# Optimization experiments

Hardware: AMD Instinct MI355X
Metric: run time of the kernel (lower is better)

## Reference

```python
import jax, jax.numpy as jnp
import numpy as np

KERNEL_MUL = 2.0
KERNEL_NUM = 5


def setup_inputs() -> dict:
    key = jax.random.key(0)
    k1, k2 = jax.random.split(key)
    N, D = 4096, 256
    source = jax.random.normal(k1, (N, D), dtype=jnp.float32)
    target = jax.random.normal(k2, (N, D), dtype=jnp.float32)
    return {"source": source, "target": target}


def _gaussian_kernel_sum(source, target):
    # total: [2N, D]
    total = jnp.concatenate([source, target], axis=0)
    n = total.shape[0]
    sq = jnp.sum(total * total, axis=1)  # [2N]
    L2 = sq[:, None] + sq[None, :] - 2.0 * (total @ total.T)  # [2N, 2N]
    # Bandwidth from detached mean of off-diagonal-normalized sum (torch uses .data)
    bandwidth = jax.lax.stop_gradient(jnp.sum(L2)) / (n * n - n)
    bandwidth = bandwidth / (KERNEL_MUL ** (KERNEL_NUM // 2))
    kernels = sum(
        jnp.exp(-L2 / (bandwidth * (KERNEL_MUL ** i))) for i in range(KERNEL_NUM)
    )
    return kernels


def reference(source, target):
    b = source.shape[0]
    K = _gaussian_kernel_sum(source, target)
    XX = jnp.mean(K[:b, :b])
    YY = jnp.mean(K[b:, b:])
    XY = jnp.mean(K[:b, b:])
    YX = jnp.mean(K[b:, :b])
    return XX + YY - XY - YX
```

## Files before the change

kernel.cpp:

```cpp
#include <hip/hip_runtime.h>


#define NROWS 8192
#define HALF  4096
#define DIM   256
#define CONVB 256
#define NTILE 2080
#define GRIDP 512

typedef float f32x4 __attribute__((ext_vector_type(4)));
typedef float f32x2 __attribute__((ext_vector_type(2)));

__device__ __forceinline__ const float* row_ptr(const float* src, const float* tgt, int r) {
    return (r < HALF) ? (src + (size_t)r * DIM) : (tgt + (size_t)(r - HALF) * DIM);
}

__device__ __forceinline__ void gload_lds16(const void* g, void* l) {
    __builtin_amdgcn_global_load_lds(
        (const __attribute__((address_space(1))) unsigned int*)g,
        (__attribute__((address_space(3))) unsigned int*)l, 16, 0, 0);
}

__device__ __forceinline__ void stage_panel(const ulonglong2* plane, int P,
                                            ulonglong2* lds, int w, int lane) {
    #pragma unroll
    for (int i = 0; i < 8; ++i) {
        int k = w + 4 * i;
        int u = k >> 1;
        int h = k & 1;
        int rg = (h * 64 + lane) ^ ((u & 3) << 1);
        gload_lds16(plane + (size_t)P * 2048 + (size_t)u * 128 + rg,
                    lds + u * 128 + h * 64);
    }
}

__global__ __launch_bounds__(256) void k_conv(const float* __restrict__ src,
                                              const float* __restrict__ tgt,
                                              unsigned char* __restrict__ hi,
                                              float* __restrict__ sq,
                                              float* __restrict__ part,
                                              double* __restrict__ parts1,
                                              float* __restrict__ outacc,
                                              unsigned int* __restrict__ cnt,
                                              float* __restrict__ out) {
    __shared__ __align__(16) unsigned char sh8[32 * 256];
    __shared__ float4 cs[4][64];
    __shared__ double s1s[4];

    int w = threadIdx.x >> 6, lane = threadIdx.x & 63;
    int r0 = blockIdx.x * 32;

    float4 v[8];
    #pragma unroll
    for (int i = 0; i < 8; ++i) {
        int row = r0 + w * 8 + i;
        v[i] = ((const float4*)row_ptr(src, tgt, row))[lane];
    }

    if (blockIdx.x == 0) {
        if (threadIdx.x < 8) outacc[threadIdx.x] = 0.0f;
        if (threadIdx.x == 0) { *cnt = 0u; out[0] = 0.0f; }
    }

    float4 csum = {0.f, 0.f, 0.f, 0.f};
    double s1w = 0.0;
    #pragma unroll
    for (int i = 0; i < 8; ++i) {
        int rl  = w * 8 + i;
        float xs[4] = {v[i].x, v[i].y, v[i].z, v[i].w};
        int pk = __builtin_amdgcn_cvt_pk_fp8_f32(xs[0], xs[1], 0, false);
        pk     = __builtin_amdgcn_cvt_pk_fp8_f32(xs[2], xs[3], pk, true);
        int o  = lane >> 1, h = lane & 1;
        *(int*)&sh8[rl * 256 + (((o ^ rl) & 31) << 3) + (h << 2)] = pk;
        csum.x += xs[0]; csum.y += xs[1]; csum.z += xs[2]; csum.w += xs[3];
        float sf = xs[0]*xs[0] + xs[1]*xs[1] + xs[2]*xs[2] + xs[3]*xs[3];
        float q0 = __builtin_amdgcn_cvt_f32_fp8(pk, 0);
        float q1 = __builtin_amdgcn_cvt_f32_fp8(pk, 1);
        float q2 = __builtin_amdgcn_cvt_f32_fp8(pk, 2);
        float q3 = __builtin_amdgcn_cvt_f32_fp8(pk, 3);
        float sQ = q0*q0 + q1*q1 + q2*q2 + q3*q3;
        #pragma unroll
        for (int off = 32; off; off >>= 1) {
            sf += __shfl_xor(sf, off, 64);
            sQ += __shfl_xor(sQ, off, 64);
        }
        if (lane == 0) { sq[r0 + rl] = sQ; s1w += (double)sf; }
    }
    __syncthreads();
    int panel = blockIdx.x >> 2, quarter = blockIdx.x & 3;
    #pragma unroll
    for (int c = threadIdx.x; c < 512; c += 256) {
        int u = c >> 5, rl = c & 31;
        int tt = u >> 2, j = u & 3;
        int o0 = 8 * tt + j;
        int o1 = 8 * tt + 4 + j;
        unsigned long long q0 = *(const unsigned long long*)
            &sh8[rl * 256 + (((o0 ^ rl) & 31) << 3)];
        unsigned long long q1 = *(const unsigned long long*)
            &sh8[rl * 256 + (((o1 ^ rl) & 31) << 3)];
        ulonglong2 q = {q0, q1};
        size_t goff = ((size_t)panel * 2048 + (size_t)u * 128 + quarter * 32 + rl);
        ((ulonglong2*)hi)[goff] = q;
    }
    cs[w][lane] = csum;
    if (lane == 0) s1s[w] = s1w;
    __syncthreads();
    if (w == 0) {
        float4 a = cs[0][lane], b = cs[1][lane], c = cs[2][lane], d = cs[3][lane];
        float4 tot = {a.x + b.x + c.x + d.x, a.y + b.y + c.y + d.y,
                      a.z + b.z + c.z + d.z, a.w + b.w + c.w + d.w};
        *(float4*)&part[(size_t)blockIdx.x * DIM + lane * 4] = tot;
        if (lane == 0) parts1[blockIdx.x] = s1s[0] + s1s[1] + s1s[2] + s1s[3];
    }
}

__global__ __launch_bounds__(256, 2) void k_pairs(const unsigned char* __restrict__ hi,
                                                  const float* __restrict__ sq,
                                                  const float* __restrict__ part,
                                                  const double* __restrict__ parts1,
                                                  float* __restrict__ outacc,
                                                  unsigned int* __restrict__ cnt,
                                                  float* __restrict__ out) {
    __shared__ __align__(16) ulonglong2 ldsA[2048];
    __shared__ __align__(16) ulonglong2 ldsB[2048];
    __shared__ float wsum[4];
    __shared__ double shd[256];

    int bid = blockIdx.x;
    int t0 = (bid * NTILE) / GRIDP;
    int t1 = ((bid + 1) * NTILE) / GRIDP;

    int id = t0, I = 0;
    for (;;) {
        int c = 64 - I;
        if (id < c) break;
        id -= c; ++I;
    }
    int J = I + id;

    int t    = threadIdx.x;
    int lane = t & 63;
    int w    = t >> 6;
    int lr   = lane & 15, lq = lane >> 4;
    int wr   = w >> 1, wc = w & 1;
    int lrx  = lr ^ (lq << 1);

    const ulonglong2* plane = (const ulonglong2*)hi;

    stage_panel(plane, I, ldsA, w, lane);
    if (J != I) stage_panel(plane, J, ldsB, w, lane);

    shd[t] = parts1[t];
    __syncthreads();
    for (int off = 128; off; off >>= 1) {
        if (t < off) shd[t] += shd[t + off];
        __syncthreads();
    }
    double S1 = shd[0];
    __syncthreads();
    {
        float c0 = 0.f, c1 = 0.f, c2 = 0.f, c3 = 0.f;
        #pragma unroll 16
        for (int b = 0; b < CONVB; b += 4) {
            c0 += part[(b + 0) * DIM + t];
            c1 += part[(b + 1) * DIM + t];
            c2 += part[(b + 2) * DIM + t];
            c3 += part[(b + 3) * DIM + t];
        }
        double c = (double)((c0 + c1) + (c2 + c3));
        shd[t] = c * c;
    }
    __syncthreads();
    for (int off = 128; off; off >>= 1) {
        if (t < off) shd[t] += shd[t + off];
        __syncthreads();
    }
    double S2    = shd[0];
    double nd    = (double)NROWS;
    double sumL2 = 2.0 * nd * S1 - 2.0 * S2;
    double bw    = sumL2 / (nd * nd - nd) / 4.0;
    float  s     = (float)(-1.0 / (16.0 * bw * 0.69314718055994530942));
    f32x2  m2s   = {-2.0f * s, -2.0f * s};

    asm volatile("s_waitcnt vmcnt(0)");
    __syncthreads();

    float wtot = 0.0f;
    int curI = I, curJ = J;

    #pragma unroll 1
    for (int tile = t0; tile < t1; ++tile) {
        const ulonglong2* lB  = (curJ == curI) ? ldsA : ldsB;
        const ulonglong2* pAl = ldsA + lq * 128 + wr * 64 + lrx;
        const ulonglong2* pBl = lB   + lq * 128 + wc * 64 + lrx;

        ulonglong2 fA[4][4], fB[4][4];
        #pragma unroll
        for (int tt = 0; tt < 4; ++tt) {
            #pragma unroll
            for (int m = 0; m < 4; ++m) fA[tt][m] = pAl[tt * 512 + m * 16];
            #pragma unroll
            for (int n = 0; n < 4; ++n) fB[tt][n] = pBl[tt * 512 + n * 16];
        }
        __syncthreads();

        int nI = curI, nJ = curJ + 1;
        if (nJ == 64) { nI = curI + 1; nJ = nI; }
        if (tile + 1 < t1) {
            if (nI != curI) stage_panel(plane, nI, ldsA, w, lane);
            else            stage_panel(plane, nJ, ldsB, w, lane);
        }

        f32x4 acc[4][4];
        #pragma unroll
        for (int m = 0; m < 4; ++m)
            #pragma unroll
            for (int n = 0; n < 4; ++n) acc[m][n] = (f32x4){0.f, 0.f, 0.f, 0.f};
        #pragma unroll
        for (int tt = 0; tt < 4; ++tt) {
            #pragma unroll
            for (int m = 0; m < 4; ++m)
                #pragma unroll
                for (int n = 0; n < 4; ++n)
                    acc[m][n] = __builtin_amdgcn_mfma_f32_16x16x32_fp8_fp8(
                        (long)fA[tt][m].x, (long)fB[tt][n].x, acc[m][n], 0, 0, 0);
            #pragma unroll
            for (int m = 0; m < 4; ++m)
                #pragma unroll
                for (int n = 0; n < 4; ++n)
                    acc[m][n] = __builtin_amdgcn_mfma_f32_16x16x32_fp8_fp8(
                        (long)fA[tt][m].y, (long)fB[tt][n].y, acc[m][n], 0, 0, 0);
        }

        float wgt = (curJ == curI) ? 1.0f : 2.0f;
        float sgn = ((curI < 32) == (curJ < 32)) ? 1.0f : -1.0f;
        int ro_eff = curI * 128 + wr * 64;
        int co_eff = curJ * 128 + wc * 64;
        float4 sqa4[4];
        float  sqbv[4];
        #pragma unroll
        for (int m = 0; m < 4; ++m) sqa4[m] = *(const float4*)&sq[ro_eff + m * 16 + lq * 4];
        #pragma unroll
        for (int n = 0; n < 4; ++n) sqbv[n] = s * sq[co_eff + n * 16 + lr];

        f32x2 ssa01[4], ssa23[4];
        #pragma unroll
        for (int m = 0; m < 4; ++m) {
            ssa01[m] = (f32x2){s * sqa4[m].x, s * sqa4[m].y};
            ssa23[m] = (f32x2){s * sqa4[m].z, s * sqa4[m].w};
        }

        f32x2 acc0 = {0.f, 0.f}, acc1 = {0.f, 0.f};
        #pragma unroll
        for (int m = 0; m < 4; ++m) {
            #pragma unroll
            for (int n = 0; n < 4; ++n) {
                f32x2 sbn = {sqbv[n], sqbv[n]};
                f32x2 a01 = {acc[m][n][0], acc[m][n][1]};
                f32x2 a23 = {acc[m][n][2], acc[m][n][3]};
                f32x2 e01 = (ssa01[m] + sbn) + m2s * a01;
                f32x2 e23 = (ssa23[m] + sbn) + m2s * a23;
                f32x2 u01, u23;
                u01.x = __builtin_amdgcn_exp2f(e01.x);
                u01.y = __builtin_amdgcn_exp2f(e01.y);
                u23.x = __builtin_amdgcn_exp2f(e23.x);
                u23.y = __builtin_amdgcn_exp2f(e23.y);
                f32x2 p2a = u01 * u01, p4a = p2a * p2a, p8a = p4a * p4a, p16a = p8a * p8a;
                f32x2 p2b = u23 * u23, p4b = p2b * p2b, p8b = p4b * p4b, p16b = p8b * p8b;
                acc0 += ((u01 + p2a) + (p4a + p8a)) + p16a;
                acc1 += ((u23 + p2b) + (p4b + p8b)) + p16b;
            }
        }
        wtot += ((acc0.x + acc0.y) + (acc1.x + acc1.y)) * sgn * wgt;

        asm volatile("s_waitcnt vmcnt(0)");
        __syncthreads();
        curI = nI; curJ = nJ;
    }

    #pragma unroll
    for (int off = 32; off; off >>= 1) wtot += __shfl_xor(wtot, off, 64);
    if (lane == 0) wsum[w] = wtot;
    __syncthreads();
    if (t == 0) {
        float tot = (wsum[0] + wsum[1] + wsum[2] + wsum[3])
                  * (1.0f / ((float)HALF * (float)HALF));
        float r = atomicAdd(&outacc[bid & 7], tot);
        asm volatile("" :: "v"(r) : "memory");
        unsigned prev = atomicAdd(cnt, 1u);
        if (prev == (unsigned)(GRIDP - 1)) {
            float total = 0.0f;
            #pragma unroll
            for (int k2 = 0; k2 < 8; ++k2) total += atomicAdd(&outacc[k2], 0.0f);
            out[0] = total;
        }
    }
}

extern "C" void kernel_launch(void* const* d_in, const int* in_sizes, int n_in,
                              void* d_out, int out_size, void* d_ws, size_t ws_size,
                              hipStream_t stream) {
    const float* src = (const float*)d_in[0];
    const float* tgt = (const float*)d_in[1];
    float* out = (float*)d_out;

    char* ws = (char*)d_ws;
    unsigned int* cnt = (unsigned int*)(ws + 0);
    float*  outacc = (float*)(ws + 64);
    float*  sq     = (float*)(ws + 128);
    float*  part   = (float*)(ws + 33024);
    double* parts1 = (double*)(ws + 295424);
    unsigned char* hi = (unsigned char*)(ws + 297472);

    k_conv <<<CONVB, 256, 0, stream>>>(src, tgt, hi, sq, part, parts1,
                                       outacc, cnt, out);
    k_pairs<<<GRIDP, 256, 0, stream>>>(hi, sq, part, parts1, outacc, cnt, out);
}
```

Before: 96.40 us.

## Software-pipeline MFMA of next tile with exp epilogue of previous tile

Restructures the tile loop so the fp8 MFMA matrix products for the current tile are interleaved with the exp-sum epilogue of the previous tile, using double accumulators (accA/accB) with a prologue and an epilogue. The aim is to overlap matrix-core work with VALU transcendental work, which previously ran back to back. Fragment loads are also split per k-step instead of loading all fragments up front. The cost is doubled accumulator register pressure (two 16x f32x4 sets), which may lower occupancy or cause spills.

```diff
diff --git a/kernel.cpp b/kernel.cpp
--- a/kernel.cpp
+++ b/kernel.cpp
@@ -187,79 +187,159 @@
 
     float wtot = 0.0f;
     int curI = I, curJ = J;
-
-    #pragma unroll 1
-    for (int tile = t0; tile < t1; ++tile) {
+    int pI = 0, pJ = 0;
+
+    f32x4 accA[4][4], accB[4][4];
+
+    {
         const ulonglong2* lB  = (curJ == curI) ? ldsA : ldsB;
         const ulonglong2* pAl = ldsA + lq * 128 + wr * 64 + lrx;
         const ulonglong2* pBl = lB   + lq * 128 + wc * 64 + lrx;
-
-        ulonglong2 fA[4][4], fB[4][4];
         #pragma unroll
         for (int tt = 0; tt < 4; ++tt) {
-            #pragma unroll
-            for (int m = 0; m < 4; ++m) fA[tt][m] = pAl[tt * 512 + m * 16];
-            #pragma unroll
-            for (int n = 0; n < 4; ++n) fB[tt][n] = pBl[tt * 512 + n * 16];
-        }
-        __syncthreads();
-
+            ulonglong2 fA[4], fB[4];
+            #pragma unroll
+            for (int m = 0; m < 4; ++m) fA[m] = pAl[tt * 512 + m * 16];
+            #pragma unroll
+            for (int n = 0; n < 4; ++n) fB[n] = pBl[tt * 512 + n * 16];
+            #pragma unroll
+            for (int m = 0; m < 4; ++m)
+                #pragma unroll
+                for (int n = 0; n < 4; ++n) {
+                    f32x4 c0 = (tt == 0) ? (f32x4){0.f,0.f,0.f,0.f} : accA[m][n];
+                    accA[m][n] = __builtin_amdgcn_mfma_f32_16x16x32_fp8_fp8(
+                        (long)fA[m].x, (long)fB[n].x, c0, 0, 0, 0);
+                }
+            #pragma unroll
+            for (int m = 0; m < 4; ++m)
+                #pragma unroll
+                for (int n = 0; n < 4; ++n)
+                    accA[m][n] = __builtin_amdgcn_mfma_f32_16x16x32_fp8_fp8(
+                        (long)fA[m].y, (long)fB[n].y, accA[m][n], 0, 0, 0);
+        }
+        __syncthreads();
+        int nI = curI, nJ = curJ + 1;
+        if (nJ == 64) { nI = curI + 1; nJ = nI; }
+        if (t0 + 1 < t1) {
+            if (nI != curI) stage_panel(plane, nI, ldsA, w, lane);
+            else            stage_panel(plane, nJ, ldsB, w, lane);
+        }
+        pI = curI; pJ = curJ; curI = nI; curJ = nJ;
+    }
+
+    #pragma unroll 1
+    for (int tile = t0 + 1; tile < t1; ++tile) {
+        asm volatile("s_waitcnt vmcnt(0)");
+        __syncthreads();
+
+        const ulonglong2* lB  = (curJ == curI) ? ldsA : ldsB;
+        const ulonglong2* pAl = ldsA + lq * 128 + wr * 64 + lrx;
+        const ulonglong2* pBl = lB   + lq * 128 + wc * 64 + lrx;
+
+        float pwgt = (pJ == pI) ? 1.0f : 2.0f;
+        float psgn = ((pI < 32) == (pJ < 32)) ? 1.0f : -1.0f;
+        int pro = pI * 128 + wr * 64;
+        int pco = pJ * 128 + wc * 64;
+        float4 sqa4[4];
+        float  psqbv[4];
+        #pragma unroll
+        for (int m = 0; m < 4; ++m) sqa4[m] = *(const float4*)&sq[pro + m * 16 + lq * 4];
+        #pragma unroll
+        for (int n = 0; n < 4; ++n) psqbv[n] = s * sq[pco + n * 16 + lr];
+        f32x2 pssa01[4], pssa23[4];
+        #pragma unroll
+        for (int m = 0; m < 4; ++m) {
+            pssa01[m] = (f32x2){s * sqa4[m].x, s * sqa4[m].y};
+            pssa23[m] = (f32x2){s * sqa4[m].z, s * sqa4[m].w};
+        }
+        f32x2 eac0 = {0.f, 0.f}, eac1 = {0.f, 0.f};
+
+        #pragma unroll
+        for (int tt = 0; tt < 4; ++tt) {
+            ulonglong2 fA[4], fB[4];
+            #pragma unroll
+            for (int m = 0; m < 4; ++m) fA[m] = pAl[tt * 512 + m * 16];
+            #pragma unroll
+            for (int n = 0; n < 4; ++n) fB[n] = pBl[tt * 512 + n * 16];
+            {
+                f32x2 sa01 = pssa01[tt], sa23 = pssa23[tt];
+                #pragma unroll
+                for (int n = 0; n < 4; ++n) {
+                    f32x2 sbn = {psqbv[n], psqbv[n]};
+                    f32x2 a01 = {accA[tt][n][0], accA[tt][n][1]};
+                    f32x2 a23 = {accA[tt][n][2], accA[tt][n][3]};
+                    f32x2 e01 = (sa01 + sbn) + m2s * a01;
+                    f32x2 e23 = (sa23 + sbn) + m2s * a23;
+                    f32x2 u01, u23;
+                    u01.x = __builtin_amdgcn_exp2f(e01.x);
+                    u01.y = __builtin_amdgcn_exp2f(e01.y);
+                    u23.x = __builtin_amdgcn_exp2f(e23.x);
+                    u23.y = __builtin_amdgcn_exp2f(e23.y);
+                    f32x2 p2a = u01 * u01, p4a = p2a * p2a, p8a = p4a * p4a, p16a = p8a * p8a;
+                    f32x2 p2b = u23 * u23, p4b = p2b * p2b, p8b = p4b * p4b, p16b = p8b * p8b;
+                    eac0 += ((u01 + p2a) + (p4a + p8a)) + p16a;
+                    eac1 += ((u23 + p2b) + (p4b + p8b)) + p16b;
+                }
+            }
+            #pragma unroll
+            for (int m = 0; m < 4; ++m)
+                #pragma unroll
+                for (int n = 0; n < 4; ++n) {
+                    f32x4 c0 = (tt == 0) ? (f32x4){0.f,0.f,0.f,0.f} : accB[m][n];
+                    accB[m][n] = __builtin_amdgcn_mfma_f32_16x16x32_fp8_fp8(
+                        (long)fA[m].x, (long)fB[n].x, c0, 0, 0, 0);
+                }
+            #pragma unroll
+            for (int m = 0; m < 4; ++m)
+                #pragma unroll
+                for (int n = 0; n < 4; ++n)
+                    accB[m][n] = __builtin_amdgcn_mfma_f32_16x16x32_fp8_fp8(
+                        (long)fA[m].y, (long)fB[n].y, accB[m][n], 0, 0, 0);
+        }
+        wtot += ((eac0.x + eac0.y) + (eac1.x + eac1.y)) * psgn * pwgt;
+
+        __syncthreads();
         int nI = curI, nJ = curJ + 1;
         if (nJ == 64) { nI = curI + 1; nJ = nI; }
         if (tile + 1 < t1) {
             if (nI != curI) stage_panel(plane, nI, ldsA, w, lane);
             else            stage_panel(plane, nJ, ldsB, w, lane);
         }
-
-        f32x4 acc[4][4];
         #pragma unroll
         for (int m = 0; m < 4; ++m)
             #pragma unroll
-            for (int n = 0; n < 4; ++n) acc[m][n] = (f32x4){0.f, 0.f, 0.f, 0.f};
-        #pragma unroll
-        for (int tt = 0; tt < 4; ++tt) {
-            #pragma unroll
-            for (int m = 0; m < 4; ++m)
-                #pragma unroll
-                for (int n = 0; n < 4; ++n)
-                    acc[m][n] = __builtin_amdgcn_mfma_f32_16x16x32_fp8_fp8(
-                        (long)fA[tt][m].x, (long)fB[tt][n].x, acc[m][n], 0, 0, 0);
-            #pragma unroll
-            for (int m = 0; m < 4; ++m)
-                #pragma unroll
-                for (int n = 0; n < 4; ++n)
-                    acc[m][n] = __builtin_amdgcn_mfma_f32_16x16x32_fp8_fp8(
-                        (long)fA[tt][m].y, (long)fB[tt][n].y, acc[m][n], 0, 0, 0);
-        }
-
-        float wgt = (curJ == curI) ? 1.0f : 2.0f;
-        float sgn = ((curI < 32) == (curJ < 32)) ? 1.0f : -1.0f;
-        int ro_eff = curI * 128 + wr * 64;
-        int co_eff = curJ * 128 + wc * 64;
+            for (int n = 0; n < 4; ++n) accA[m][n] = accB[m][n];
+        pI = curI; pJ = curJ; curI = nI; curJ = nJ;
+    }
+
+    {
+        float pwgt = (pJ == pI) ? 1.0f : 2.0f;
+        float psgn = ((pI < 32) == (pJ < 32)) ? 1.0f : -1.0f;
+        int pro = pI * 128 + wr * 64;
+        int pco = pJ * 128 + wc * 64;
         float4 sqa4[4];
-        float  sqbv[4];
-        #pragma unroll
-        for (int m = 0; m < 4; ++m) sqa4[m] = *(const float4*)&sq[ro_eff + m * 16 + lq * 4];
-        #pragma unroll
-        for (int n = 0; n < 4; ++n) sqbv[n] = s * sq[co_eff + n * 16 + lr];
-
-        f32x2 ssa01[4], ssa23[4];
+        float  psqbv[4];
+        #pragma unroll
+        for (int m = 0; m < 4; ++m) sqa4[m] = *(const float4*)&sq[pro + m * 16 + lq * 4];
+        #pragma unroll
+        for (int n = 0; n < 4; ++n) psqbv[n] = s * sq[pco + n * 16 + lr];
+        f32x2 pssa01[4], pssa23[4];
         #pragma unroll
         for (int m = 0; m < 4; ++m) {
-            ssa01[m] = (f32x2){s * sqa4[m].x, s * sqa4[m].y};
-            ssa23[m] = (f32x2){s * sqa4[m].z, s * sqa4[m].w};
-        }
-
-        f32x2 acc0 = {0.f, 0.f}, acc1 = {0.f, 0.f};
+            pssa01[m] = (f32x2){s * sqa4[m].x, s * sqa4[m].y};
+            pssa23[m] = (f32x2){s * sqa4[m].z, s * sqa4[m].w};
+        }
+        f32x2 eac0 = {0.f, 0.f}, eac1 = {0.f, 0.f};
         #pragma unroll
         for (int m = 0; m < 4; ++m) {
+            f32x2 sa01 = pssa01[m], sa23 = pssa23[m];
             #pragma unroll
             for (int n = 0; n < 4; ++n) {
-                f32x2 sbn = {sqbv[n], sqbv[n]};
-                f32x2 a01 = {acc[m][n][0], acc[m][n][1]};
-                f32x2 a23 = {acc[m][n][2], acc[m][n][3]};
-                f32x2 e01 = (ssa01[m] + sbn) + m2s * a01;
-                f32x2 e23 = (ssa23[m] + sbn) + m2s * a23;
+                f32x2 sbn = {psqbv[n], psqbv[n]};
+                f32x2 a01 = {accA[m][n][0], accA[m][n][1]};
+                f32x2 a23 = {accA[m][n][2], accA[m][n][3]};
+                f32x2 e01 = (sa01 + sbn) + m2s * a01;
+                f32x2 e23 = (sa23 + sbn) + m2s * a23;
                 f32x2 u01, u23;
                 u01.x = __builtin_amdgcn_exp2f(e01.x);
                 u01.y = __builtin_amdgcn_exp2f(e01.y);
@@ -267,15 +347,11 @@
                 u23.y = __builtin_amdgcn_exp2f(e23.y);
                 f32x2 p2a = u01 * u01, p4a = p2a * p2a, p8a = p4a * p4a, p16a = p8a * p8a;
                 f32x2 p2b = u23 * u23, p4b = p2b * p2b, p8b = p4b * p4b, p16b = p8b * p8b;
-                acc0 += ((u01 + p2a) + (p4a + p8a)) + p16a;
-                acc1 += ((u23 + p2b) + (p4b + p8b)) + p16b;
+                eac0 += ((u01 + p2a) + (p4a + p8a)) + p16a;
+                eac1 += ((u23 + p2b) + (p4b + p8b)) + p16b;
             }
         }
-        wtot += ((acc0.x + acc0.y) + (acc1.x + acc1.y)) * sgn * wgt;
-
-        asm volatile("s_waitcnt vmcnt(0)");
-        __syncthreads();
-        curI = nI; curJ = nJ;
+        wtot += ((eac0.x + eac0.y) + (eac1.x + eac1.y)) * psgn * pwgt;
     }
 
     #pragma unroll
```

After: 95.96 us. No clear change (-0.5%).
